# Kernel tuning notes

Hardware: AMD Instinct MI355X
Metric: run time of the kernel (lower is better)

Reference implementation:

```python
import jax, jax.numpy as jnp
import numpy as np

N = 4096
IN_DIM = 256
HID = 64
NHEADS = 4
OUT_DIM = 128
ALPHA = 0.5  # LeakyReLU negative slope
NEG_INF = -9e15


def gat_layer(x, mask, W, a, concat):
    """Dense GraphAttentionLayer (pyGAT style).
    x:[N,Fin], mask:[N,N] bool, W:[Fin,Fout], a:[2*Fout]."""
    Wh = x @ W                                   # [N, Fout]
    Fout = W.shape[1]
    f1 = Wh @ a[:Fout]                           # [N]
    f2 = Wh @ a[Fout:]                           # [N]
    e = jax.nn.leaky_relu(f1[:, None] + f2[None, :], negative_slope=ALPHA)  # [N,N]
    att = jax.nn.softmax(jnp.where(mask, e, NEG_INF), axis=1)               # [N,N]
    h = att @ Wh                                 # [N, Fout]
    return jax.nn.elu(h) if concat else h


def setup_inputs() -> dict:
    key = jax.random.key(0)
    ks = jax.random.split(key, 6)
    x = jax.random.normal(ks[0], (N, IN_DIM), dtype=jnp.float32)
    adj = jax.random.randint(ks[1], (N, N), 0, 2, dtype=jnp.int32)
    s_in = 1.0 / np.sqrt(IN_DIM)
    s_hid = 1.0 / np.sqrt(HID * NHEADS)
    W_heads = jax.random.uniform(ks[2], (NHEADS, IN_DIM, HID), jnp.float32, -s_in, s_in)
    a_heads = jax.random.uniform(ks[3], (NHEADS, 2 * HID), jnp.float32, -s_in, s_in)
    W_out = jax.random.uniform(ks[4], (HID * NHEADS, OUT_DIM), jnp.float32, -s_hid, s_hid)
    a_out = jax.random.uniform(ks[5], (2 * OUT_DIM,), jnp.float32, -s_hid, s_hid)
    return {"x": x, "adj": adj, "W_heads": W_heads, "a_heads": a_heads,
            "W_out": W_out, "a_out": a_out}


def reference(x, adj, W_heads, a_heads, W_out, a_out):
    mask = adj > 0
    # multi-head attention, concat along feature dim
    heads = jax.vmap(lambda W, a: gat_layer(x, mask, W, a, True))(W_heads, a_heads)
    h = jnp.transpose(heads, (1, 0, 2)).reshape(N, NHEADS * HID)  # [N, H*HID]
    # dropout=0 -> identity; final GAT layer (concat=False) + outer ELU
    out = jax.nn.elu(gat_layer(h, mask, W_out, a_out, False))     # [N, OUT_DIM]
    return out
```

## Files before the change

### kernel.cpp

```cpp
#include <hip/hip_runtime.h>
#include <hip/hip_bf16.h>

#define N 4096
#define IN_DIM 256
#define HID 64
#define NHEADS 4
#define OUT_DIM 128
#define LOG2E 1.44269504088896340736f

typedef __attribute__((ext_vector_type(8))) short bf16x8;
typedef __attribute__((ext_vector_type(4))) float f32x4;

__global__ __launch_bounds__(256, 4) void prep_kernel(
        const float* __restrict__ x, const float* __restrict__ W,
        const float* __restrict__ a, const int* __restrict__ adj,
        __hip_bfloat16* __restrict__ WhB,
        float* __restrict__ f1, float* __restrict__ f2,
        unsigned* __restrict__ maskT) {
    __shared__ float xs[8 * IN_DIM];
    const int t = threadIdx.x;
    if (blockIdx.x < 512) {
        const int c = t & 63, h = t >> 6;
        const int i0 = blockIdx.x * 8;
        const float4* xg = (const float4*)(x + (size_t)i0 * IN_DIM);
        float4* xs4 = (float4*)xs;
        for (int u = t; u < 8 * IN_DIM / 4; u += 256) xs4[u] = xg[u];
        __syncthreads();
        float acc[8];
#pragma unroll
        for (int r = 0; r < 8; r++) acc[r] = 0.f;
        const float* Wp = W + (size_t)h * IN_DIM * HID + c;
        for (int k = 0; k < IN_DIM; k += 4) {
            const float w0 = Wp[(size_t)(k + 0) * HID];
            const float w1 = Wp[(size_t)(k + 1) * HID];
            const float w2 = Wp[(size_t)(k + 2) * HID];
            const float w3 = Wp[(size_t)(k + 3) * HID];
#pragma unroll
            for (int r = 0; r < 8; r++) {
                const float4 xv = *(const float4*)(xs + r * IN_DIM + k);
                acc[r] += xv.x * w0 + xv.y * w1 + xv.z * w2 + xv.w * w3;
            }
        }
        union { ushort u[8]; uint4 v; } cv;
#pragma unroll
        for (int r = 0; r < 8; r++)
            cv.u[r] = __hip_bfloat16_raw(__float2bfloat16(acc[r])).x;
        const int jblk = i0 >> 5, quad = (i0 >> 3) & 3;
        const int lane_idx = (c & 15) + 16 * quad;
        *(uint4*)(WhB + ((((size_t)h * (N / 32) + jblk) * 4 + (c >> 4)) * 64 +
                         lane_idx) * 8) = cv.v;
        const float av1 = a[h * 2 * HID + c];
        const float av2 = a[h * 2 * HID + HID + c];
        float s1[8], s2[8];
#pragma unroll
        for (int r = 0; r < 8; r++) { s1[r] = acc[r] * av1; s2[r] = acc[r] * av2; }
#pragma unroll
        for (int mm = 32; mm > 0; mm >>= 1) {
#pragma unroll
            for (int r = 0; r < 8; r++) {
                s1[r] += __shfl_xor(s1[r], mm, 64);
                s2[r] += __shfl_xor(s2[r], mm, 64);
            }
        }
        if (c == 0) {
#pragma unroll
            for (int r = 0; r < 8; r++) {
                f1[(size_t)h * N + i0 + r] = s1[r] * LOG2E;
                f2[(size_t)h * N + i0 + r] = s2[r] * LOG2E;
            }
        }
    } else {
        const int lane = t & 63, w = t >> 6;
        const int i = (blockIdx.x - 512) * 4 + w;
        const int4* arow = (const int4*)(adj + (size_t)i * N);
        for (int jb = 0; jb < N / 256; jb++) {
            const int4 a4 = arow[jb * 64 + lane];
            unsigned long long bal[4];
            bal[0] = __ballot(a4.x > 0);
            bal[1] = __ballot(a4.y > 0);
            bal[2] = __ballot(a4.z > 0);
            bal[3] = __ballot(a4.w > 0);
            if (lane < 8) {
                unsigned word = 0;
#pragma unroll
                for (int e = 0; e < 4; e++) {
                    unsigned xv = (unsigned)(bal[e] >> (8 * lane)) & 0xFFu;
                    xv = (xv | (xv << 12)) & 0x000F000Fu;
                    xv = (xv | (xv << 6))  & 0x03030303u;
                    xv = (xv | (xv << 3))  & 0x11111111u;
                    word |= xv << e;
                }
                maskT[(size_t)(jb * 8 + lane) * N + i] = word;
            }
        }
    }
}

template <int HEADS, int D, int DSL, int G, int MW>
__global__ __launch_bounds__(G * 64, 4) void attn_fused(
        const unsigned* __restrict__ maskT,
        const __hip_bfloat16* __restrict__ WhB,
        const float* __restrict__ f1g, const float* __restrict__ f2g,
        float* __restrict__ outp) {
    constexpr int CTtot = D / 16;
    constexpr int CTT = CTtot / DSL;
    constexpr int CC = (D == 64) ? 1 : 2;
    constexpr int KSTEPS = N / (32 * G);
    __shared__ float sh[MW * G * 16 * CC * 17];
    __shared__ float dsh[MW * G * 16];
    const int t = threadIdx.x;
    const int g = t >> 6, lane = t & 63;
    const int m = lane & 15, quad = lane >> 4;
    const int h = blockIdx.y / DSL, slc = blockIdx.y % DSL;
    const int i0 = blockIdx.x * (16 * MW);

    float f1v[MW];
#pragma unroll
    for (int mw = 0; mw < MW; mw++)
        f1v[mw] = f1g[(size_t)h * N + i0 + mw * 16 + m];
    const float* f2p = f2g + (size_t)h * N;
    const bf16x8* whb = (const bf16x8*)WhB + (size_t)h * (N / 32) * CTtot * 64;

    const f32x4 zero = {0.f, 0.f, 0.f, 0.f};
    f32x4 acc[MW][CTT];
    f32x4 sac[MW];
#pragma unroll
    for (int mw = 0; mw < MW; mw++) {
        sac[mw] = zero;
#pragma unroll
        for (int ct = 0; ct < CTT; ct++) acc[mw][ct] = zero;
    }
    const short one_bf = (short)0x3F80;
    const bf16x8 ones = {one_bf, one_bf, one_bf, one_bf,
                         one_bf, one_bf, one_bf, one_bf};

    unsigned mwrd[2][MW];
    float f2v[2][8];
    auto stage_mf = [&](int ks, int b) {
        const int j0 = g * (N / G) + ks * 32;
        const int jw = j0 >> 5;
#pragma unroll
        for (int mw = 0; mw < MW; mw++)
            mwrd[b][mw] = maskT[(size_t)jw * N + i0 + mw * 16 + m];
        const float4 lo = *(const float4*)(f2p + j0 + quad * 8);
        const float4 hi = *(const float4*)(f2p + j0 + quad * 8 + 4);
        f2v[b][0] = lo.x; f2v[b][1] = lo.y; f2v[b][2] = lo.z; f2v[b][3] = lo.w;
        f2v[b][4] = hi.x; f2v[b][5] = hi.y; f2v[b][6] = hi.z; f2v[b][7] = hi.w;
    };

    stage_mf(0, 0);
#pragma unroll 2
    for (int ks = 0; ks < KSTEPS; ks++) {
        const int cur = ks & 1;
        const int jwc = (g * (N / G) + ks * 32) >> 5;
        const bf16x8* bp = whb + ((size_t)jwc * CTtot + slc * CTT) * 64 + lane;
        bf16x8 bfrag[CTT];
#pragma unroll
        for (int ct = 0; ct < CTT; ct++) bfrag[ct] = bp[ct * 64];
        if (ks + 1 < KSTEPS) stage_mf(ks + 1, cur ^ 1);
        bf16x8 afr[MW];
#pragma unroll
        for (int mw = 0; mw < MW; mw++) {
            const unsigned mword = mwrd[cur][mw] >> (quad * 8);
            float p[8];
#pragma unroll
            for (int e = 0; e < 8; e++) {
                const float tt = f1v[mw] + f2v[cur][e];
                const float lr = fmaxf(tt, 0.5f * tt);
                const float pe = __builtin_amdgcn_exp2f(lr);
                p[e] = ((mword >> e) & 1u) ? pe : 0.f;
            }
            union { bf16x8 v; __hip_bfloat162 h2[4]; } u;
#pragma unroll
            for (int e2 = 0; e2 < 4; e2++)
                u.h2[e2] = __float22bfloat162_rn(
                    make_float2(p[2 * e2], p[2 * e2 + 1]));
            afr[mw] = u.v;
        }
#pragma unroll
        for (int ct = 0; ct < CTT; ct++)
#pragma unroll
            for (int mw = 0; mw < MW; mw++)
                acc[mw][ct] = __builtin_amdgcn_mfma_f32_16x16x32_bf16(
                    afr[mw], bfrag[ct], acc[mw][ct], 0, 0, 0);
#pragma unroll
        for (int mw = 0; mw < MW; mw++)
            sac[mw] = __builtin_amdgcn_mfma_f32_16x16x32_bf16(
                afr[mw], ones, sac[mw], 0, 0, 0);
    }

#pragma unroll
    for (int rd = 0; rd < CTT / CC; rd++) {
#pragma unroll
        for (int mw = 0; mw < MW; mw++) {
#pragma unroll
            for (int cc = 0; cc < CC; cc++) {
#pragma unroll
                for (int r = 0; r < 4; r++)
                    sh[(((mw * G + g) * 16 + quad * 4 + r) * CC + cc) * 17 + m] =
                        acc[mw][rd * CC + cc][r];
            }
            if (rd == 0 && m == 0) {
#pragma unroll
                for (int r = 0; r < 4; r++)
                    dsh[(mw * G + g) * 16 + quad * 4 + r] = sac[mw][r];
            }
        }
        __syncthreads();
        if (t < 16 * CC * 16) {
            int row, chl;
            if (D == 64) { row = t & 15; chl = (t >> 4) & 15; }
            else         { chl = t & 31; row = (t >> 5) & 15; }
#pragma unroll
            for (int mw = 0; mw < MW; mw++) {
                float av = 0.f, ss = 0.f;
#pragma unroll
                for (int gg = 0; gg < G; gg++) {
                    av += sh[(((mw * G + gg) * 16 + row) * CC + (chl >> 4)) * 17 +
                             (chl & 15)];
                    ss += dsh[(mw * G + gg) * 16 + row];
                }
                float v = av / ss;
                v = (v > 0.f) ? v : (__builtin_amdgcn_exp2f(v * LOG2E) - 1.f);
                const int chg = h * D + slc * (CTT * 16) + rd * CC * 16 + chl;
                const int irow = i0 + mw * 16 + row;
                if (D == 64)
                    outp[(size_t)chg * N + irow] = v;
                else
                    outp[(size_t)irow * D + chg] = v;
            }
        }
        __syncthreads();
    }
}

__global__ void gemm2_kernel(const float* __restrict__ h1T,
                             const float* __restrict__ W2,
                             const float* __restrict__ a2,
                             __hip_bfloat16* __restrict__ WhB2,
                             float* __restrict__ f1, float* __restrict__ f2) {
    __shared__ float hs[8 * IN_DIM];
    __shared__ float fred[2][2][4][2];
    const int t = threadIdx.x;
    const int c = t & 127, rh = t >> 7;
    const int i0 = blockIdx.x * 8;
    for (int u = t; u < 8 * IN_DIM; u += 256) {
        const int r = u & 7, k = u >> 3;
        hs[r * IN_DIM + k] = h1T[(size_t)k * N + i0 + r];
    }
    __syncthreads();
    float acc[4];
#pragma unroll
    for (int rr = 0; rr < 4; rr++) acc[rr] = 0.f;
    for (int k = 0; k < IN_DIM; k += 4) {
        const float w0 = W2[(size_t)(k + 0) * OUT_DIM + c];
        const float w1 = W2[(size_t)(k + 1) * OUT_DIM + c];
        const float w2 = W2[(size_t)(k + 2) * OUT_DIM + c];
        const float w3 = W2[(size_t)(k + 3) * OUT_DIM + c];
#pragma unroll
        for (int rr = 0; rr < 4; rr++) {
            const float4 hv = *(const float4*)(hs + (rh * 4 + rr) * IN_DIM + k);
            acc[rr] += hv.x * w0 + hv.y * w1 + hv.z * w2 + hv.w * w3;
        }
    }
    union { ushort u[4]; uint2 v; } cv;
#pragma unroll
    for (int rr = 0; rr < 4; rr++)
        cv.u[rr] = __hip_bfloat16_raw(__float2bfloat16(acc[rr])).x;
    const int jblk = i0 >> 5, quad = (i0 >> 3) & 3;
    const int lane_idx = (c & 15) + 16 * quad;
    *(uint2*)((__hip_bfloat16*)WhB2 +
              (((size_t)jblk * 8 + (c >> 4)) * 64 + lane_idx) * 8 + rh * 4) = cv.v;
    const float av1 = a2[c], av2 = a2[OUT_DIM + c];
    float s1[4], s2[4];
#pragma unroll
    for (int rr = 0; rr < 4; rr++) { s1[rr] = acc[rr] * av1; s2[rr] = acc[rr] * av2; }
#pragma unroll
    for (int mm = 32; mm > 0; mm >>= 1) {
#pragma unroll
        for (int rr = 0; rr < 4; rr++) {
            s1[rr] += __shfl_xor(s1[rr], mm, 64);
            s2[rr] += __shfl_xor(s2[rr], mm, 64);
        }
    }
    if ((t & 63) == 0) {
        const int chalf = (t >> 6) & 1;
#pragma unroll
        for (int rr = 0; rr < 4; rr++) {
            fred[rh][chalf][rr][0] = s1[rr];
            fred[rh][chalf][rr][1] = s2[rr];
        }
    }
    __syncthreads();
    if (t < 16) {
        const int fn = t & 1, rr = (t >> 1) & 3, rh2 = t >> 3;
        const float v = (fred[rh2][0][rr][fn] + fred[rh2][1][rr][fn]) * LOG2E;
        (fn ? f2 : f1)[i0 + rh2 * 4 + rr] = v;
    }
}

extern "C" void kernel_launch(void* const* d_in, const int* in_sizes, int n_in,
                              void* d_out, int out_size, void* d_ws, size_t ws_size,
                              hipStream_t stream) {
    const float* x   = (const float*)d_in[0];
    const int*   adj = (const int*)d_in[1];
    const float* Wh_ = (const float*)d_in[2];
    const float* ah  = (const float*)d_in[3];
    const float* W2  = (const float*)d_in[4];
    const float* a2  = (const float*)d_in[5];
    float* out = (float*)d_out;

    float* ws = (float*)d_ws;
    float* f1a = ws;
    float* f2a = f1a + (size_t)NHEADS * N;
    float* f1b = f2a + (size_t)NHEADS * N;
    float* f2b = f1b + N;
    float* h1T = f2b + N;
    __hip_bfloat16* WhB1 = (__hip_bfloat16*)(h1T + (size_t)IN_DIM * N);
    __hip_bfloat16* WhB2 = WhB1 + (size_t)NHEADS * HID * N;
    unsigned* maskT = (unsigned*)(WhB2 + (size_t)OUT_DIM * N);

    prep_kernel<<<1536, 256, 0, stream>>>(x, Wh_, ah, adj, WhB1, f1a, f2a, maskT);
    attn_fused<NHEADS, HID, 1, 8, 2>
        <<<dim3(N / 32, NHEADS), 512, 0, stream>>>(maskT, WhB1, f1a, f2a, h1T);
    gemm2_kernel<<<N / 8, 256, 0, stream>>>(h1T, W2, a2, WhB2, f1b, f2b);
    attn_fused<1, OUT_DIM, 2, 8, 1>
        <<<dim3(N / 16, 2), 512, 0, stream>>>(maskT, WhB2, f1b, f2b, out);
}
```

Measured before the change: 185.7 us.

## Drop LDS staging in projection GEMMs and use single channel slice for layer two

The prep and second-layer projection kernels now read x and h1T straight from global memory instead of staging them in shared memory behind a barrier. gemm2 gets launch bounds and a simpler per-k loop over float4 row groups. The final attention launch changes from two channel slices to one, halving its grid while each block covers all output channels. This removes LDS traffic and syncs, at the cost of more redundant global or cache reads and less parallelism in the last attention stage.

```diff
diff --git a/kernel.cpp b/kernel.cpp
--- a/kernel.cpp
+++ b/kernel.cpp
@@ -17,19 +17,16 @@
         __hip_bfloat16* __restrict__ WhB,
         float* __restrict__ f1, float* __restrict__ f2,
         unsigned* __restrict__ maskT) {
-    __shared__ float xs[8 * IN_DIM];
     const int t = threadIdx.x;
     if (blockIdx.x < 512) {
         const int c = t & 63, h = t >> 6;
         const int i0 = blockIdx.x * 8;
-        const float4* xg = (const float4*)(x + (size_t)i0 * IN_DIM);
-        float4* xs4 = (float4*)xs;
-        for (int u = t; u < 8 * IN_DIM / 4; u += 256) xs4[u] = xg[u];
-        __syncthreads();
+        const float* xb = x + (size_t)i0 * IN_DIM;
         float acc[8];
 #pragma unroll
         for (int r = 0; r < 8; r++) acc[r] = 0.f;
         const float* Wp = W + (size_t)h * IN_DIM * HID + c;
+#pragma unroll 2
         for (int k = 0; k < IN_DIM; k += 4) {
             const float w0 = Wp[(size_t)(k + 0) * HID];
             const float w1 = Wp[(size_t)(k + 1) * HID];
@@ -37,7 +34,7 @@
             const float w3 = Wp[(size_t)(k + 3) * HID];
 #pragma unroll
             for (int r = 0; r < 8; r++) {
-                const float4 xv = *(const float4*)(xs + r * IN_DIM + k);
+                const float4 xv = *(const float4*)(xb + r * IN_DIM + k);
                 acc[r] += xv.x * w0 + xv.y * w1 + xv.z * w2 + xv.w * w3;
             }
         }
@@ -234,34 +231,25 @@
     }
 }
 
-__global__ void gemm2_kernel(const float* __restrict__ h1T,
-                             const float* __restrict__ W2,
-                             const float* __restrict__ a2,
-                             __hip_bfloat16* __restrict__ WhB2,
-                             float* __restrict__ f1, float* __restrict__ f2) {
-    __shared__ float hs[8 * IN_DIM];
+__global__ __launch_bounds__(256, 4) void gemm2_kernel(
+        const float* __restrict__ h1T, const float* __restrict__ W2,
+        const float* __restrict__ a2, __hip_bfloat16* __restrict__ WhB2,
+        float* __restrict__ f1, float* __restrict__ f2) {
     __shared__ float fred[2][2][4][2];
     const int t = threadIdx.x;
     const int c = t & 127, rh = t >> 7;
     const int i0 = blockIdx.x * 8;
-    for (int u = t; u < 8 * IN_DIM; u += 256) {
-        const int r = u & 7, k = u >> 3;
-        hs[r * IN_DIM + k] = h1T[(size_t)k * N + i0 + r];
-    }
-    __syncthreads();
+    const float* hb = h1T + i0 + rh * 4;
+    const float* w2p = W2 + c;
     float acc[4];
 #pragma unroll
     for (int rr = 0; rr < 4; rr++) acc[rr] = 0.f;
-    for (int k = 0; k < IN_DIM; k += 4) {
-        const float w0 = W2[(size_t)(k + 0) * OUT_DIM + c];
-        const float w1 = W2[(size_t)(k + 1) * OUT_DIM + c];
-        const float w2 = W2[(size_t)(k + 2) * OUT_DIM + c];
-        const float w3 = W2[(size_t)(k + 3) * OUT_DIM + c];
-#pragma unroll
-        for (int rr = 0; rr < 4; rr++) {
-            const float4 hv = *(const float4*)(hs + (rh * 4 + rr) * IN_DIM + k);
-            acc[rr] += hv.x * w0 + hv.y * w1 + hv.z * w2 + hv.w * w3;
-        }
+#pragma unroll 4
+    for (int k = 0; k < IN_DIM; k++) {
+        const float4 hv = *(const float4*)(hb + (size_t)k * N);
+        const float wv = w2p[(size_t)k * OUT_DIM];
+        acc[0] += hv.x * wv; acc[1] += hv.y * wv;
+        acc[2] += hv.z * wv; acc[3] += hv.w * wv;
     }
     union { ushort u[4]; uint2 v; } cv;
 #pragma unroll
@@ -324,6 +312,6 @@
     attn_fused<NHEADS, HID, 1, 8, 2>
         <<<dim3(N / 32, NHEADS), 512, 0, stream>>>(maskT, WhB1, f1a, f2a, h1T);
     gemm2_kernel<<<N / 8, 256, 0, stream>>>(h1T, W2, a2, WhB2, f1b, f2b);
-    attn_fused<1, OUT_DIM, 2, 8, 1>
-        <<<dim3(N / 16, 2), 512, 0, stream>>>(maskT, WhB2, f1b, f2b, out);
+    attn_fused<1, OUT_DIM, 1, 8, 1>
+        <<<dim3(N / 16, 1), 512, 0, stream>>>(maskT, WhB2, f1b, f2b, out);
 }
```

Measured after the change: 212.3 us. 14.3% more time.
